# Optimization experiments

Measured on AMD Instinct MI355X. Metric: run time of the kernel, lower is better.

## Reference

```python
import jax, jax.numpy as jnp
import numpy as np

B, L, D = 4, 2048, 512
CHUNK = 64
EPS = 1e-5


def setup_inputs() -> dict:
    key = jax.random.key(0)
    kx, kw = jax.random.split(key)
    x = jax.random.normal(kx, (B, L, D), dtype=jnp.float32)
    W = jax.random.normal(kw, (D, D), dtype=jnp.float32) / np.float32(np.sqrt(D))
    return {
        "x": x,
        "W": W,
        "eta": jnp.asarray(0.01, jnp.float32),
        "lam_logit": jnp.asarray(np.log(0.99 / 0.01), jnp.float32),  # logit(0.99)
        "ln_gamma": jnp.ones((D,), jnp.float32),
        "ln_beta": jnp.zeros((D,), jnp.float32),
    }


def _gated_delta_scan(k, v, q, lam, beta):
    """Gated delta rule: S_t = lam*S_{t-1} + beta * k_t (x) (v_t - lam*S_{t-1}^T k_t);
    o_t = S_t^T q_t (scale=1.0, single head of dim D). k,v,q: [B,L,D] -> o: [B,L,D]."""
    b, l, d = k.shape
    nc = l // CHUNK

    def to_scan(t):  # [B,L,D] -> [nc, CHUNK, B, D]
        return t.transpose(1, 0, 2).reshape(nc, CHUNK, b, d)

    ks, vs, qs = to_scan(k), to_scan(v), to_scan(q)

    def step(S, inp):
        k_t, v_t, q_t = inp                      # each [B,D]
        S = lam * S                              # scalar decay exp(g), g = log(lam)
        v_err = beta * (v_t - jnp.einsum('bk,bkv->bv', k_t, S))
        S = S + k_t[:, :, None] * v_err[:, None, :]
        o_t = jnp.einsum('bk,bkv->bv', q_t, S)
        return S, o_t

    def chunk_body(S, ch):
        return jax.lax.scan(step, S, ch)

    S0 = jnp.zeros((b, d, d), k.dtype)
    _, o = jax.lax.scan(chunk_body, S0, (ks, vs, qs))  # o: [nc, CHUNK, B, D]
    return o.reshape(l, b, d).transpose(1, 0, 2)


def reference(x, W, eta, lam_logit, ln_gamma, ln_beta):
    lam = jax.nn.sigmoid(lam_logit)
    x_act = jnp.tanh(x)
    static_out = jnp.einsum('bld,ed->ble', x_act, W)  # torch Linear (no bias): x @ W.T
    # k = q = tanh(x), v = W @ tanh(x), g = log(lam), beta = eta
    o_dyn = _gated_delta_scan(x_act, static_out, x_act, lam, eta)
    y = static_out + o_dyn
    mu = jnp.mean(y, axis=-1, keepdims=True)
    var = jnp.var(y, axis=-1, keepdims=True)
    return (y - mu) * jax.lax.rsqrt(var + EPS) * ln_gamma + ln_beta
```

## Files before the change

kernel.cpp:

```cpp
#include <hip/hip_runtime.h>
#include <math.h>

#define BB 4
#define LL 2048
#define DD 512
#define CC 64
#define NC 32
#define VB 8
#define EPSF 1e-5f

typedef unsigned int u32;
typedef unsigned short u16;
typedef __attribute__((ext_vector_type(4))) u32 u32x4;
typedef __attribute__((ext_vector_type(4))) float f32x4;
typedef __attribute__((ext_vector_type(8))) __bf16 bf16x8;

__device__ __forceinline__ u16 f2bf(float f) {
  return __builtin_bit_cast(u16, (__bf16)f);
}
__device__ __forceinline__ int sx6(int s) { return (s ^ (s >> 3)) & 7; }
__device__ __forceinline__ bf16x8 ldf(const u16* p) {
  return __builtin_bit_cast(bf16x8, *(const u32x4*)p);
}
__device__ __forceinline__ bf16x8 bcv(u32x4 v) { return __builtin_bit_cast(bf16x8, v); }

__device__ __forceinline__ void gld16(u16* lds, const u16* g) {
  __builtin_amdgcn_global_load_lds(
      (const __attribute__((address_space(1))) u32*)g,
      (__attribute__((address_space(3))) u32*)lds, 16, 0, 0);
}
__device__ __forceinline__ void barrier_lgkm() {
  asm volatile("s_waitcnt lgkmcnt(0)" ::: "memory");
  __builtin_amdgcn_sched_barrier(0);
  __builtin_amdgcn_s_barrier();
  __builtin_amdgcn_sched_barrier(0);
}
__device__ __forceinline__ void barrier_all() {
  asm volatile("s_waitcnt vmcnt(0) lgkmcnt(0)" ::: "memory");
  __builtin_amdgcn_sched_barrier(0);
  __builtin_amdgcn_s_barrier();
  __builtin_amdgcn_sched_barrier(0);
}

__global__ __launch_bounds__(256) void k_pre2(const float* __restrict__ x,
                                              const float* __restrict__ W,
                                              u16* __restrict__ kbs,
                                              u16* __restrict__ wbb,
                                              u16* __restrict__ kbt) {
  __shared__ __align__(16) u16 Ls[16 * 520];
  int blk = blockIdx.x;
  int tid = threadIdx.x;
  if (blk < 512) {
    int bc = blk >> 2;
    int q = blk & 3;
    int b = bc >> 5, c = bc & 31;
    int s0 = q * 16;
    const float* xg = x + (size_t)(b * LL + c * CC + s0) * DD;
    u16* kbs_c = kbs + (size_t)(b * LL + c * CC + s0) * DD;
#pragma unroll
    for (int i = 0; i < 4; ++i) {
      int idx = tid + i * 256;
      int r = idx >> 6, k8 = (idx & 63) * 8;
      const float* xp = xg + (size_t)r * DD + k8;
      float4 a = *(const float4*)xp;
      float4 b4 = *(const float4*)(xp + 4);
      float v[8] = {a.x, a.y, a.z, a.w, b4.x, b4.y, b4.z, b4.w};
      u32x4 pk;
#pragma unroll
      for (int j = 0; j < 4; ++j)
        pk[j] = (u32)f2bf(tanhf(v[2 * j])) | ((u32)f2bf(tanhf(v[2 * j + 1])) << 16);
      int s = s0 + r;
      *(u32x4*)(kbs_c + (size_t)r * DD + (k8 ^ (sx6(s) << 3))) = pk;
      *(u32x4*)&Ls[r * 520 + k8] = pk;
    }
    __syncthreads();
    u16* ktb = kbt + (size_t)bc * CC * DD;
#pragma unroll
    for (int kk = 0; kk < 2; ++kk) {
      int k = tid * 2 + kk;
      int mk = sx6(k) << 3;
#pragma unroll
      for (int g2 = 0; g2 < 2; ++g2) {
        int g = q * 2 + g2;
        u32 w4[4];
#pragma unroll
        for (int p = 0; p < 4; ++p) {
          int sL = g2 * 8 + 2 * p;
          u16 e0 = Ls[sL * 520 + k];
          u16 e1 = Ls[(sL + 1) * 520 + k];
          w4[p] = (u32)e0 | ((u32)e1 << 16);
        }
        *(u32x4*)(ktb + (size_t)k * 64 + ((8 * g) ^ mk)) =
            (u32x4){w4[0], w4[1], w4[2], w4[3]};
      }
    }
  } else {
    int idx = ((blk - 512) * 256 + tid) * 8;
    float4 a = *(const float4*)(W + idx);
    float4 b = *(const float4*)(W + idx + 4);
    float v[8] = {a.x, a.y, a.z, a.w, b.x, b.y, b.z, b.w};
    u32x4 pk;
#pragma unroll
    for (int j = 0; j < 4; ++j)
      pk[j] = (u32)f2bf(v[2 * j]) | ((u32)f2bf(v[2 * j + 1]) << 16);
    *(u32x4*)(wbb + idx) = pk;
  }
}

__global__ __launch_bounds__(512) void k_prep5(const u16* __restrict__ kbs,
                                               const float* __restrict__ eta_p,
                                               const float* __restrict__ ll_p,
                                               u16* __restrict__ tbs,
                                               u16* __restrict__ tcs,
                                               u16* __restrict__ p1g,
                                               u16* __restrict__ p2g) {
  __shared__ __align__(16) u16 Kl[CC * DD];
  __shared__ float Gl[64 * 64];
  __shared__ float Gs[64 * 64];
  __shared__ float Tl[64 * 65];
  __shared__ __align__(16) u16 MtL[64 * 64];
  __shared__ __align__(16) u16 TbT[64 * 64];
  __shared__ __align__(16) u16 TcT[64 * 64];
  __shared__ float pw[72];
  int bc = blockIdx.x;
  int b = bc >> 5, c = bc & 31;
  int tid = threadIdx.x;
  int wid = tid >> 6, lane = tid & 63;
  int wq2 = wid & 3, kh2 = wid >> 2;
  int lo = lane & 15, hi = lane >> 4;
  float beta = *eta_p;
  float lam = 1.f / (1.f + expf(-*ll_p));
  if (tid <= 64) pw[tid] = powf(lam, (float)tid);
  for (int i = tid; i < 64 * 65; i += 512) Tl[i] = 0.f;
  const u16* Kg = kbs + (size_t)(b * LL + c * CC) * DD;
#pragma unroll
  for (int i = 0; i < 8; ++i)
    gld16(Kl + (size_t)(i * 512 + tid) * 8, Kg + (size_t)(i * 512 + tid) * 8);
  __syncthreads();
  {
    f32x4 acc[4] = {{0.f,0.f,0.f,0.f},{0.f,0.f,0.f,0.f},{0.f,0.f,0.f,0.f},{0.f,0.f,0.f,0.f}};
    int t = 16 * wq2 + lo;
    int mT = sx6(t) << 3;
#pragma unroll
    for (int kq = 0; kq < 8; ++kq) {
      int col = kh2 * 256 + hi * 8 + kq * 32;
      bf16x8 aF = ldf(Kl + t * DD + (col ^ mT));
#pragma unroll
      for (int sb = 0; sb < 4; ++sb) {
        int s = 16 * sb + lo;
        bf16x8 bF = ldf(Kl + s * DD + (col ^ (sx6(s) << 3)));
        acc[sb] = __builtin_amdgcn_mfma_f32_16x16x32_bf16(aF, bF, acc[sb], 0, 0, 0);
      }
    }
    float* Gp = kh2 ? Gs : Gl;
#pragma unroll
    for (int sb = 0; sb < 4; ++sb)
#pragma unroll
      for (int r = 0; r < 4; ++r)
        Gp[(16 * wq2 + 4 * hi + r) * 64 + 16 * sb + lo] = acc[sb][r];
  }
  __syncthreads();
#pragma unroll
  for (int i = 0; i < 8; ++i) {
    int idx = tid + i * 512;
    int tq = idx >> 6, sq = idx & 63;
    float g = Gl[idx] + Gs[idx];
    Gl[idx] = g;
    Gs[idx] = (sq < tq) ? beta * pw[tq - sq] * g : 0.f;
  }
  __syncthreads();
  if (tid < 256) {
    int q = hi;
    int j = 16 * wid + lo;
    for (int t = 0; t < 64; ++t) {
      float ps = 0.f;
#pragma unroll
      for (int i = 0; i < 16; ++i) {
        int s = 16 * q + i;
        ps = fmaf(Gs[t * 64 + s], Tl[s * 65 + j], ps);
      }
      ps += __shfl_xor(ps, 16, 64);
      ps += __shfl_xor(ps, 32, 64);
      if (q == 0) Tl[t * 65 + j] = ((t == j) ? 1.f : 0.f) - ps;
    }
  }
  __syncthreads();
  u16* tbso = tbs + (size_t)bc * 4096;
  u16* tcso = tcs + (size_t)bc * 4096;
#pragma unroll
  for (int i = 0; i < 8; ++i) {
    int idx = tid + i * 512;
    int s = idx >> 6, r = idx & 63;
    float tv = Tl[s * 65 + r];
    float sc = pw[63 - s] * beta;
    tbso[idx] = f2bf(sc * tv);
    tcso[idx] = f2bf(-sc * pw[r + 1] * tv);
    int swz = r ^ (sx6(s) << 3);
    float mtv = (r < s) ? pw[s - r] * Gl[s * 64 + r]
                        : ((r == s) ? Gl[s * 64 + r] : 0.f);
    MtL[s * 64 + swz] = f2bf(mtv);
    float tvT = Tl[r * 65 + s];
    TbT[s * 64 + swz] = f2bf(beta * tvT);
    TcT[s * 64 + swz] = f2bf(-beta * pw[s + 1] * tvT);
  }
  __syncthreads();
  {
    f32x4 pa[4];
#pragma unroll
    for (int rt = 0; rt < 4; ++rt) pa[rt] = (f32x4){0.f, 0.f, 0.f, 0.f};
    int srow = 16 * wq2 + lo;
    int aswz = sx6(srow) << 3;
    const u16* Bt = kh2 ? TcT : TbT;
#pragma unroll
    for (int km = 0; km < 2; ++km) {
      int mo = hi * 8 + km * 32;
      bf16x8 aF = ldf(MtL + srow * 64 + (mo ^ aswz));
#pragma unroll
      for (int rt = 0; rt < 4; ++rt) {
        int rrow = 16 * rt + lo;
        int bswz = sx6(rrow) << 3;
        pa[rt] = __builtin_amdgcn_mfma_f32_16x16x32_bf16(
            aF, ldf(Bt + rrow * 64 + (mo ^ bswz)), pa[rt], 0, 0, 0);
      }
    }
    u16* po = (kh2 ? p2g : p1g) + (size_t)bc * 4096;
#pragma unroll
    for (int rt = 0; rt < 4; ++rt)
#pragma unroll
      for (int rg = 0; rg < 4; ++rg) {
        int s = 16 * wq2 + 4 * hi + rg;
        int r = 16 * rt + lo;
        float d = kh2 ? ((s == r) ? pw[s + 1] : 0.f)
                      : ((s == r) ? 1.f : 0.f);
        po[s * 64 + r] = f2bf(pa[rt][rg] + d);
      }
  }
}

__global__ __launch_bounds__(512, 2) void k_scanC(const u16* __restrict__ kbs,
                                                  const u16* __restrict__ kbt,
                                                  const u16* __restrict__ wbb,
                                                  const u16* __restrict__ tbs,
                                                  const u16* __restrict__ tcs,
                                                  const u16* __restrict__ p1g,
                                                  const u16* __restrict__ p2g,
                                                  const float* __restrict__ ll_p,
                                                  float* __restrict__ y) {
  __shared__ __align__(16) u16 Sb[16 * DD];
  __shared__ __align__(16) u16 Ut2[2][16 * 64];
  __shared__ __align__(16) u16 Vt2[2][16 * 64];
  __shared__ __align__(16) u16 Ws[16 * 64];

  int b = blockIdx.x >> 6;
  int vb = blockIdx.x & 63;
  int v0 = vb * VB;
  int tid = threadIdx.x;
  int wid = tid >> 6, lane = tid & 63;
  int wq = wid & 3, kh = wid >> 2;
  int lo = lane & 15, hi = lane >> 4;
  int sidx = 16 * wq + lo;
  int mS = sx6(sidx) << 3;
  int mLo = sx6(lo) << 3;
  int kOff = kh * 256;

  float lam = 1.f / (1.f + expf(-*ll_p));
  float lam64 = powf(lam, 64.f);

  {
    u32x4 z = {0u, 0u, 0u, 0u};
    ((u32x4*)Sb)[tid] = z;
    if (tid < 256) {
      ((u32x4*)Ut2)[tid] = z;
      ((u32x4*)Vt2)[tid] = z;
    }
    if (tid < 128) ((u32x4*)Ws)[tid] = z;
    if (wid < 8) {
      u32x4 wrow = *(const u32x4*)(wbb + (size_t)(v0 + wid) * DD + lane * 8);
      *(u32x4*)(Sb + (size_t)(8 + wid) * DD + ((lane * 8) ^ (sx6(8 + wid) << 3))) = wrow;
    }
  }
  const u16* kb_b = kbs + (size_t)b * LL * DD;
  float* yb = y + (size_t)b * LL * DD;

  u32x4 kB[8];
#pragma unroll
  for (int kq = 0; kq < 8; ++kq)
    kB[kq] = *(const u32x4*)(kb_b + (size_t)sidx * DD +
                             ((kOff + hi * 8 + kq * 32) ^ mS));
  u32x4 kt0[4], kt1[4], fA0, fA1, fB0, fB1;
  {
    const u16* ktc = kbt + (size_t)(b * NC + 0) * CC * DD;
#pragma unroll
    for (int t = 0; t < 4; ++t) {
      int k = 16 * (4 * wid + t) + lo;
      const u16* rowp = ktc + (size_t)k * 64;
      int m = sx6(k) << 3;
      kt0[t] = *(const u32x4*)(rowp + ((8 * hi) ^ m));
      kt1[t] = *(const u32x4*)(rowp + ((8 * hi + 32) ^ m));
    }
    size_t tbase = ((size_t)(b * NC + 0) * 64 + sidx) * 64 + hi * 8;
    const u16* mA = (kh == 0) ? tbs : p1g;
    const u16* mB = (kh == 0) ? tcs : p2g;
    fA0 = *(const u32x4*)(mA + tbase);
    fA1 = *(const u32x4*)(mA + tbase + 32);
    fB0 = *(const u32x4*)(mB + tbase);
    fB1 = *(const u32x4*)(mB + tbase + 32);
  }
  f32x4 Sa[4];
#pragma unroll
  for (int t = 0; t < 4; ++t) Sa[t] = (f32x4){0.f, 0.f, 0.f, 0.f};
  barrier_all();

  for (int c = 0; c < NC; ++c) {
    {
      f32x4 A0 = {0.f,0.f,0.f,0.f}, A1 = {0.f,0.f,0.f,0.f};
#pragma unroll
      for (int kq = 0; kq < 8; ++kq) {
        int col = kOff + hi * 8 + kq * 32;
        bf16x8 sA = ldf(Sb + lo * DD + (col ^ mLo));
        if (kq & 1) A1 = __builtin_amdgcn_mfma_f32_16x16x32_bf16(sA, bcv(kB[kq]), A1, 0, 0, 0);
        else        A0 = __builtin_amdgcn_mfma_f32_16x16x32_bf16(sA, bcv(kB[kq]), A0, 0, 0, 0);
      }
      f32x4 F = A0 + A1;
      if (hi < 2) {
#pragma unroll
        for (int r = 0; r < 4; ++r) {
          int m = 4 * hi + r;
          Ut2[kh][m * 64 + (sidx ^ (sx6(m) << 3))] = f2bf(F[r]);
        }
      } else {
#pragma unroll
        for (int r = 0; r < 4; ++r) {
          int m = 4 * hi + r - 8;
          Vt2[kh][m * 64 + (sidx ^ (sx6(m) << 3))] = f2bf(F[r]);
        }
      }
    }
    if (c + 1 < NC) {
      const u16* src = kb_b + ((size_t)(c + 1) * CC + sidx) * DD;
#pragma unroll
      for (int kq = 0; kq < 8; ++kq)
        kB[kq] = *(const u32x4*)(src + ((kOff + hi * 8 + kq * 32) ^ mS));
    }
    barrier_lgkm();
    {
      f32x4 Wa0 = {0.f,0.f,0.f,0.f}, Wa1 = {0.f,0.f,0.f,0.f};
#pragma unroll
      for (int h = 0; h < 2; ++h) {
        bf16x8 vf0 = ldf(Vt2[h] + lo * 64 + ((hi * 8) ^ mLo));
        bf16x8 vf1 = ldf(Vt2[h] + lo * 64 + ((hi * 8 + 32) ^ mLo));
        bf16x8 uf0 = ldf(Ut2[h] + lo * 64 + ((hi * 8) ^ mLo));
        bf16x8 uf1 = ldf(Ut2[h] + lo * 64 + ((hi * 8 + 32) ^ mLo));
        Wa0 = __builtin_amdgcn_mfma_f32_16x16x32_bf16(vf0, bcv(fA0), Wa0, 0, 0, 0);
        Wa1 = __builtin_amdgcn_mfma_f32_16x16x32_bf16(vf1, bcv(fA1), Wa1, 0, 0, 0);
        Wa0 = __builtin_amdgcn_mfma_f32_16x16x32_bf16(uf0, bcv(fB0), Wa0, 0, 0, 0);
        Wa1 = __builtin_amdgcn_mfma_f32_16x16x32_bf16(uf1, bcv(fB1), Wa1, 0, 0, 0);
      }
      f32x4 Wa = Wa0 + Wa1;
      if (kh == 0) {
        if (hi < 2) {
#pragma unroll
          for (int r = 0; r < 4; ++r) {
            int v = 4 * hi + r;
            Ws[v * 64 + (sidx ^ (sx6(v) << 3))] = f2bf(Wa[r]);
          }
        }
      } else {
        if (hi < 2) {
          float4 yo = make_float4(Wa[0], Wa[1], Wa[2], Wa[3]);
          *(float4*)(yb + (size_t)(c * CC + sidx) * DD + v0 + 4 * hi) = yo;
        }
      }
    }
    barrier_lgkm();
    {
      bf16x8 ws0 = ldf(Ws + lo * 64 + ((hi * 8) ^ mLo));
      bf16x8 ws1 = ldf(Ws + lo * 64 + ((hi * 8 + 32) ^ mLo));
#pragma unroll
      for (int t = 0; t < 4; ++t) {
        f32x4 acc = Sa[t] * lam64;
        acc = __builtin_amdgcn_mfma_f32_16x16x32_bf16(ws0, bcv(kt0[t]), acc, 0, 0, 0);
        acc = __builtin_amdgcn_mfma_f32_16x16x32_bf16(ws1, bcv(kt1[t]), acc, 0, 0, 0);
        Sa[t] = acc;
      }
      if (hi < 2) {
#pragma unroll
        for (int t = 0; t < 4; ++t) {
          int kc = 16 * (4 * wid + t) + lo;
#pragma unroll
          for (int r = 0; r < 4; ++r) {
            int v = 4 * hi + r;
            Sb[v * DD + (kc ^ (sx6(v) << 3))] = f2bf(Sa[t][r]);
          }
        }
      }
    }
    if (c + 1 < NC) {
      const u16* ktc = kbt + (size_t)(b * NC + c + 1) * CC * DD;
#pragma unroll
      for (int t = 0; t < 4; ++t) {
        int k = 16 * (4 * wid + t) + lo;
        const u16* rowp = ktc + (size_t)k * 64;
        int m = sx6(k) << 3;
        kt0[t] = *(const u32x4*)(rowp + ((8 * hi) ^ m));
        kt1[t] = *(const u32x4*)(rowp + ((8 * hi + 32) ^ m));
      }
      size_t tbase = ((size_t)(b * NC + c + 1) * 64 + sidx) * 64 + hi * 8;
      const u16* mA = (kh == 0) ? tbs : p1g;
      const u16* mB = (kh == 0) ? tcs : p2g;
      fA0 = *(const u32x4*)(mA + tbase);
      fA1 = *(const u32x4*)(mA + tbase + 32);
      fB0 = *(const u32x4*)(mB + tbase);
      fB1 = *(const u32x4*)(mB + tbase + 32);
    }
    barrier_lgkm();
  }
}

__global__ __launch_bounds__(256) void k_ln(float* __restrict__ y,
                                            const float* __restrict__ gamma,
                                            const float* __restrict__ lbeta) {
  int row = blockIdx.x * 4 + (threadIdx.x >> 6);
  int lane = threadIdx.x & 63;
  float* yr = y + (size_t)row * DD + lane * 8;
  float4 a = *(const float4*)yr;
  float4 b = *(const float4*)(yr + 4);
  float v[8] = {a.x, a.y, a.z, a.w, b.x, b.y, b.z, b.w};
  float s = 0.f, ss = 0.f;
#pragma unroll
  for (int j = 0; j < 8; ++j) {
    s += v[j];
    ss = fmaf(v[j], v[j], ss);
  }
#pragma unroll
  for (int m = 1; m < 64; m <<= 1) {
    s += __shfl_xor(s, m, 64);
    ss += __shfl_xor(ss, m, 64);
  }
  float mu = s * (1.f / DD);
  float var = ss * (1.f / DD) - mu * mu;
  float inv = rsqrtf(var + EPSF);
  const float* gp = gamma + lane * 8;
  const float* bp = lbeta + lane * 8;
  float4 g0 = *(const float4*)gp;
  float4 g1 = *(const float4*)(gp + 4);
  float4 b0 = *(const float4*)bp;
  float4 b1 = *(const float4*)(bp + 4);
  float g[8] = {g0.x, g0.y, g0.z, g0.w, g1.x, g1.y, g1.z, g1.w};
  float bb[8] = {b0.x, b0.y, b0.z, b0.w, b1.x, b1.y, b1.z, b1.w};
#pragma unroll
  for (int j = 0; j < 8; ++j) v[j] = (v[j] - mu) * inv * g[j] + bb[j];
  *(float4*)yr = make_float4(v[0], v[1], v[2], v[3]);
  *(float4*)(yr + 4) = make_float4(v[4], v[5], v[6], v[7]);
}

extern "C" void kernel_launch(void* const* d_in, const int* in_sizes, int n_in,
                              void* d_out, int out_size, void* d_ws, size_t ws_size,
                              hipStream_t stream) {
  const float* x     = (const float*)d_in[0];
  const float* W     = (const float*)d_in[1];
  const float* eta   = (const float*)d_in[2];
  const float* ll    = (const float*)d_in[3];
  const float* gamma = (const float*)d_in[4];
  const float* lbeta = (const float*)d_in[5];
  float* out = (float*)d_out;

  u16* kbs = (u16*)d_ws;
  u16* kbt = kbs + (size_t)BB * LL * DD;
  u16* wbb = kbt + (size_t)BB * LL * DD;
  u16* tbs = wbb + (size_t)DD * DD;
  u16* tcs = tbs + (size_t)BB * NC * 64 * 64;
  u16* p1g = tcs + (size_t)BB * NC * 64 * 64;
  u16* p2g = p1g + (size_t)BB * NC * 64 * 64;

  k_pre2<<<640, 256, 0, stream>>>(x, W, kbs, wbb, kbt);
  k_prep5<<<BB * NC, 512, 0, stream>>>(kbs, eta, ll, tbs, tcs, p1g, p2g);
  k_scanC<<<256, 512, 0, stream>>>(kbs, kbt, wbb, tbs, tcs, p1g, p2g, ll, out);
  k_ln<<<2048, 256, 0, stream>>>(out, gamma, lbeta);
}
```

Baseline: 131.3 us.

## Process chunk pairs per scan iteration with precomputed cross-chunk correction matrices

The sequential scan now advances two 64-token chunks per iteration. The second chunk's output takes a correction term built from the first chunk's W via extra matrices (tgg/pgg), which the prep kernel computes for odd chunks using a cross-chunk K·K^T product. The state update then runs once per pair with lam^128 decay. This halves the number of serial state updates and their barriers. The cost is more registers, shared memory, prep work and extra bf16 rounding in the correction path.

```diff
diff --git a/kernel.cpp b/kernel.cpp
--- a/kernel.cpp
+++ b/kernel.cpp
@@ -6,6 +6,7 @@
 #define DD 512
 #define CC 64
 #define NC 32
+#define NP 16
 #define VB 8
 #define EPSF 1e-5f
 
@@ -107,13 +108,15 @@
   }
 }
 
-__global__ __launch_bounds__(512) void k_prep5(const u16* __restrict__ kbs,
+__global__ __launch_bounds__(512) void k_prep6(const u16* __restrict__ kbs,
                                                const float* __restrict__ eta_p,
                                                const float* __restrict__ ll_p,
                                                u16* __restrict__ tbs,
                                                u16* __restrict__ tcs,
                                                u16* __restrict__ p1g,
-                                               u16* __restrict__ p2g) {
+                                               u16* __restrict__ p2g,
+                                               u16* __restrict__ tgg,
+                                               u16* __restrict__ pgg) {
   __shared__ __align__(16) u16 Kl[CC * DD];
   __shared__ float Gl[64 * 64];
   __shared__ float Gs[64 * 64];
@@ -122,8 +125,12 @@
   __shared__ __align__(16) u16 TbT[64 * 64];
   __shared__ __align__(16) u16 TcT[64 * 64];
   __shared__ float pw[72];
+  u16* TcsA = (u16*)Gs;
+  u16* GxT  = (u16*)Gs + 4096;
+  u16* P2A  = (u16*)Gl;
   int bc = blockIdx.x;
   int b = bc >> 5, c = bc & 31;
+  int odd = c & 1;
   int tid = threadIdx.x;
   int wid = tid >> 6, lane = tid & 63;
   int wq2 = wid & 3, kh2 = wid >> 2;
@@ -185,6 +192,8 @@
     }
   }
   __syncthreads();
+  float lam64 = pw[64];
+  float cscl = odd ? lam64 : 1.f;
   u16* tbso = tbs + (size_t)bc * 4096;
   u16* tcso = tcs + (size_t)bc * 4096;
 #pragma unroll
@@ -193,8 +202,9 @@
     int s = idx >> 6, r = idx & 63;
     float tv = Tl[s * 65 + r];
     float sc = pw[63 - s] * beta;
+    float tcv = -sc * pw[r + 1] * tv;
     tbso[idx] = f2bf(sc * tv);
-    tcso[idx] = f2bf(-sc * pw[r + 1] * tv);
+    tcso[idx] = f2bf(cscl * tcv);
     int swz = r ^ (sx6(s) << 3);
     float mtv = (r < s) ? pw[s - r] * Gl[s * 64 + r]
                         : ((r == s) ? Gl[s * 64 + r] : 0.f);
@@ -202,6 +212,7 @@
     float tvT = Tl[r * 65 + s];
     TbT[s * 64 + swz] = f2bf(beta * tvT);
     TcT[s * 64 + swz] = f2bf(-beta * pw[s + 1] * tvT);
+    if (odd) TcsA[s * 64 + swz] = f2bf(tcv);
   }
   __syncthreads();
   {
@@ -232,24 +243,89 @@
         int r = 16 * rt + lo;
         float d = kh2 ? ((s == r) ? pw[s + 1] : 0.f)
                       : ((s == r) ? 1.f : 0.f);
-        po[s * 64 + r] = f2bf(pa[rt][rg] + d);
-      }
-  }
-}
-
-__global__ __launch_bounds__(512, 2) void k_scanC(const u16* __restrict__ kbs,
+        float val = pa[rt][rg] + d;
+        po[s * 64 + r] = f2bf(kh2 ? (cscl * val) : val);
+        if (odd && kh2)
+          P2A[s * 64 + ((16 * rt + lo) ^ (sx6(s) << 3))] = f2bf(val);
+      }
+  }
+  if (odd) {
+    const u16* K0g = kbs + (size_t)(b * LL + (c - 1) * CC) * DD;
+#pragma unroll
+    for (int blk2 = 0; blk2 < 2; ++blk2) {
+      int idx = 2 * wid + blk2;
+      int qb = idx >> 2, rb = idx & 3;
+      int qrow = qb * 16 + lo;
+      int rrow = rb * 16 + lo;
+      int mQ = sx6(qrow) << 3;
+      int mR = sx6(rrow) << 3;
+      f32x4 acc = (f32x4){0.f, 0.f, 0.f, 0.f};
+#pragma unroll
+      for (int km = 0; km < 16; ++km) {
+        int col = hi * 8 + km * 32;
+        bf16x8 aF = ldf(Kl + qrow * DD + (col ^ mQ));
+        bf16x8 bF = ldf(K0g + (size_t)rrow * DD + (col ^ mR));
+        acc = __builtin_amdgcn_mfma_f32_16x16x32_bf16(aF, bF, acc, 0, 0, 0);
+      }
+#pragma unroll
+      for (int rr = 0; rr < 4; ++rr) {
+        int qv = qb * 16 + 4 * hi + rr;
+        int rv = rb * 16 + lo;
+        GxT[rv * 64 + (qv ^ (sx6(rv) << 3))] = f2bf(acc[rr]);
+      }
+    }
+    __syncthreads();
+    {
+      f32x4 pa[4];
+#pragma unroll
+      for (int rt = 0; rt < 4; ++rt) pa[rt] = (f32x4){0.f, 0.f, 0.f, 0.f};
+      int srow = 16 * wq2 + lo;
+      int aswz = sx6(srow) << 3;
+      const u16* At = kh2 ? P2A : TcsA;
+#pragma unroll
+      for (int km = 0; km < 2; ++km) {
+        int mo = hi * 8 + km * 32;
+        bf16x8 aF = ldf(At + srow * 64 + (mo ^ aswz));
+#pragma unroll
+        for (int rt = 0; rt < 4; ++rt) {
+          int rrow = 16 * rt + lo;
+          int bswz = sx6(rrow) << 3;
+          pa[rt] = __builtin_amdgcn_mfma_f32_16x16x32_bf16(
+              aF, ldf(GxT + rrow * 64 + (mo ^ bswz)), pa[rt], 0, 0, 0);
+        }
+      }
+      u16* po = (kh2 ? pgg : tgg) + (size_t)(b * NP + (c >> 1)) * 4096;
+#pragma unroll
+      for (int rt = 0; rt < 4; ++rt)
+#pragma unroll
+        for (int rg = 0; rg < 4; ++rg) {
+          int s = 16 * wq2 + 4 * hi + rg;
+          int r = 16 * rt + lo;
+          po[s * 64 + r] = f2bf(pa[rt][rg]);
+        }
+    }
+  }
+}
+
+__global__ __launch_bounds__(512, 2) void k_scanD(const u16* __restrict__ kbs,
                                                   const u16* __restrict__ kbt,
                                                   const u16* __restrict__ wbb,
                                                   const u16* __restrict__ tbs,
                                                   const u16* __restrict__ tcs,
                                                   const u16* __restrict__ p1g,
                                                   const u16* __restrict__ p2g,
+                                                  const u16* __restrict__ tgg,
+                                                  const u16* __restrict__ pgg,
                                                   const float* __restrict__ ll_p,
                                                   float* __restrict__ y) {
   __shared__ __align__(16) u16 Sb[16 * DD];
-  __shared__ __align__(16) u16 Ut2[2][16 * 64];
-  __shared__ __align__(16) u16 Vt2[2][16 * 64];
-  __shared__ __align__(16) u16 Ws[16 * 64];
+  __shared__ __align__(16) u16 Ut0[2][16 * 64];
+  __shared__ __align__(16) u16 Vt0[2][16 * 64];
+  __shared__ __align__(16) u16 Ut1[2][16 * 64];
+  __shared__ __align__(16) u16 Vt1[2][16 * 64];
+  __shared__ __align__(16) u16 Ws0[16 * 64];
+  __shared__ __align__(16) u16 Ws0s[16 * 64];
+  __shared__ __align__(16) u16 Ws1[16 * 64];
 
   int b = blockIdx.x >> 6;
   int vb = blockIdx.x & 63;
@@ -265,15 +341,22 @@
 
   float lam = 1.f / (1.f + expf(-*ll_p));
   float lam64 = powf(lam, 64.f);
+  float lam128 = lam64 * lam64;
 
   {
     u32x4 z = {0u, 0u, 0u, 0u};
     ((u32x4*)Sb)[tid] = z;
     if (tid < 256) {
-      ((u32x4*)Ut2)[tid] = z;
-      ((u32x4*)Vt2)[tid] = z;
-    }
-    if (tid < 128) ((u32x4*)Ws)[tid] = z;
+      ((u32x4*)Ut0)[tid] = z;
+      ((u32x4*)Vt0)[tid] = z;
+      ((u32x4*)Ut1)[tid] = z;
+      ((u32x4*)Vt1)[tid] = z;
+    }
+    if (tid < 128) {
+      ((u32x4*)Ws0)[tid] = z;
+      ((u32x4*)Ws0s)[tid] = z;
+      ((u32x4*)Ws1)[tid] = z;
+    }
     if (wid < 8) {
       u32x4 wrow = *(const u32x4*)(wbb + (size_t)(v0 + wid) * DD + lane * 8);
       *(u32x4*)(Sb + (size_t)(8 + wid) * DD + ((lane * 8) ^ (sx6(8 + wid) << 3))) = wrow;
@@ -282,79 +365,102 @@
   const u16* kb_b = kbs + (size_t)b * LL * DD;
   float* yb = y + (size_t)b * LL * DD;
 
-  u32x4 kB[8];
-#pragma unroll
-  for (int kq = 0; kq < 8; ++kq)
-    kB[kq] = *(const u32x4*)(kb_b + (size_t)sidx * DD +
-                             ((kOff + hi * 8 + kq * 32) ^ mS));
-  u32x4 kt0[4], kt1[4], fA0, fA1, fB0, fB1;
+  u32x4 kB0[8], kB1[8];
+#pragma unroll
+  for (int kq = 0; kq < 8; ++kq) {
+    int col = (kOff + hi * 8 + kq * 32) ^ mS;
+    kB0[kq] = *(const u32x4*)(kb_b + (size_t)sidx * DD + col);
+    kB1[kq] = *(const u32x4*)(kb_b + (size_t)(CC + sidx) * DD + col);
+  }
+  u32x4 kt0a[4], kt0b[4], kt1a[4], kt1b[4];
+  u32x4 f2A0, f2A1, f2B0, f2B1, f3A0, f3A1, f3B0, f3B1, f3G0, f3G1;
   {
-    const u16* ktc = kbt + (size_t)(b * NC + 0) * CC * DD;
+    const u16* kc0 = kbt + (size_t)(b * NC + 0) * CC * DD;
+    const u16* kc1 = kbt + (size_t)(b * NC + 1) * CC * DD;
 #pragma unroll
     for (int t = 0; t < 4; ++t) {
       int k = 16 * (4 * wid + t) + lo;
-      const u16* rowp = ktc + (size_t)k * 64;
       int m = sx6(k) << 3;
-      kt0[t] = *(const u32x4*)(rowp + ((8 * hi) ^ m));
-      kt1[t] = *(const u32x4*)(rowp + ((8 * hi + 32) ^ m));
-    }
-    size_t tbase = ((size_t)(b * NC + 0) * 64 + sidx) * 64 + hi * 8;
-    const u16* mA = (kh == 0) ? tbs : p1g;
-    const u16* mB = (kh == 0) ? tcs : p2g;
-    fA0 = *(const u32x4*)(mA + tbase);
-    fA1 = *(const u32x4*)(mA + tbase + 32);
-    fB0 = *(const u32x4*)(mB + tbase);
-    fB1 = *(const u32x4*)(mB + tbase + 32);
+      kt0a[t] = *(const u32x4*)(kc0 + (size_t)k * 64 + ((8 * hi) ^ m));
+      kt0b[t] = *(const u32x4*)(kc0 + (size_t)k * 64 + ((8 * hi + 32) ^ m));
+      kt1a[t] = *(const u32x4*)(kc1 + (size_t)k * 64 + ((8 * hi) ^ m));
+      kt1b[t] = *(const u32x4*)(kc1 + (size_t)k * 64 + ((8 * hi + 32) ^ m));
+    }
+    size_t t2 = ((size_t)(b * NC + 0) * 64 + sidx) * 64 + hi * 8;
+    size_t t3 = ((size_t)(b * NC + 1) * 64 + sidx) * 64 + hi * 8;
+    size_t tg = ((size_t)(b * NP + 0) * 64 + sidx) * 64 + hi * 8;
+    const u16* mA = kh ? p1g : tbs;
+    const u16* mB = kh ? p2g : tcs;
+    const u16* mG = kh ? pgg : tgg;
+    f2A0 = *(const u32x4*)(mA + t2); f2A1 = *(const u32x4*)(mA + t2 + 32);
+    f2B0 = *(const u32x4*)(mB + t2); f2B1 = *(const u32x4*)(mB + t2 + 32);
+    f3A0 = *(const u32x4*)(mA + t3); f3A1 = *(const u32x4*)(mA + t3 + 32);
+    f3B0 = *(const u32x4*)(mB + t3); f3B1 = *(const u32x4*)(mB + t3 + 32);
+    f3G0 = *(const u32x4*)(mG + tg); f3G1 = *(const u32x4*)(mG + tg + 32);
   }
   f32x4 Sa[4];
 #pragma unroll
   for (int t = 0; t < 4; ++t) Sa[t] = (f32x4){0.f, 0.f, 0.f, 0.f};
   barrier_all();
 
-  for (int c = 0; c < NC; ++c) {
+  for (int p = 0; p < NP; ++p) {
     {
       f32x4 A0 = {0.f,0.f,0.f,0.f}, A1 = {0.f,0.f,0.f,0.f};
+      f32x4 C0 = {0.f,0.f,0.f,0.f}, C1 = {0.f,0.f,0.f,0.f};
 #pragma unroll
       for (int kq = 0; kq < 8; ++kq) {
         int col = kOff + hi * 8 + kq * 32;
         bf16x8 sA = ldf(Sb + lo * DD + (col ^ mLo));
-        if (kq & 1) A1 = __builtin_amdgcn_mfma_f32_16x16x32_bf16(sA, bcv(kB[kq]), A1, 0, 0, 0);
-        else        A0 = __builtin_amdgcn_mfma_f32_16x16x32_bf16(sA, bcv(kB[kq]), A0, 0, 0, 0);
-      }
-      f32x4 F = A0 + A1;
+        if (kq & 1) {
+          A1 = __builtin_amdgcn_mfma_f32_16x16x32_bf16(sA, bcv(kB0[kq]), A1, 0, 0, 0);
+          C1 = __builtin_amdgcn_mfma_f32_16x16x32_bf16(sA, bcv(kB1[kq]), C1, 0, 0, 0);
+        } else {
+          A0 = __builtin_amdgcn_mfma_f32_16x16x32_bf16(sA, bcv(kB0[kq]), A0, 0, 0, 0);
+          C0 = __builtin_amdgcn_mfma_f32_16x16x32_bf16(sA, bcv(kB1[kq]), C0, 0, 0, 0);
+        }
+      }
+      f32x4 F0 = A0 + A1, F1 = C0 + C1;
       if (hi < 2) {
 #pragma unroll
         for (int r = 0; r < 4; ++r) {
           int m = 4 * hi + r;
-          Ut2[kh][m * 64 + (sidx ^ (sx6(m) << 3))] = f2bf(F[r]);
+          int off = m * 64 + (sidx ^ (sx6(m) << 3));
+          Ut0[kh][off] = f2bf(F0[r]);
+          Ut1[kh][off] = f2bf(F1[r]);
         }
       } else {
 #pragma unroll
         for (int r = 0; r < 4; ++r) {
           int m = 4 * hi + r - 8;
-          Vt2[kh][m * 64 + (sidx ^ (sx6(m) << 3))] = f2bf(F[r]);
-        }
-      }
-    }
-    if (c + 1 < NC) {
-      const u16* src = kb_b + ((size_t)(c + 1) * CC + sidx) * DD;
-#pragma unroll
-      for (int kq = 0; kq < 8; ++kq)
-        kB[kq] = *(const u32x4*)(src + ((kOff + hi * 8 + kq * 32) ^ mS));
+          int off = m * 64 + (sidx ^ (sx6(m) << 3));
+          Vt0[kh][off] = f2bf(F0[r]);
+          Vt1[kh][off] = f2bf(F1[r]);
+        }
+      }
+    }
+    if (p + 1 < NP) {
+      const u16* s0 = kb_b + ((size_t)(2 * p + 2) * CC + sidx) * DD;
+      const u16* s1 = kb_b + ((size_t)(2 * p + 3) * CC + sidx) * DD;
+#pragma unroll
+      for (int kq = 0; kq < 8; ++kq) {
+        int col = (kOff + hi * 8 + kq * 32) ^ mS;
+        kB0[kq] = *(const u32x4*)(s0 + col);
+        kB1[kq] = *(const u32x4*)(s1 + col);
+      }
     }
     barrier_lgkm();
     {
       f32x4 Wa0 = {0.f,0.f,0.f,0.f}, Wa1 = {0.f,0.f,0.f,0.f};
 #pragma unroll
       for (int h = 0; h < 2; ++h) {
-        bf16x8 vf0 = ldf(Vt2[h] + lo * 64 + ((hi * 8) ^ mLo));
-        bf16x8 vf1 = ldf(Vt2[h] + lo * 64 + ((hi * 8 + 32) ^ mLo));
-        bf16x8 uf0 = ldf(Ut2[h] + lo * 64 + ((hi * 8) ^ mLo));
-        bf16x8 uf1 = ldf(Ut2[h] + lo * 64 + ((hi * 8 + 32) ^ mLo));
-        Wa0 = __builtin_amdgcn_mfma_f32_16x16x32_bf16(vf0, bcv(fA0), Wa0, 0, 0, 0);
-        Wa1 = __builtin_amdgcn_mfma_f32_16x16x32_bf16(vf1, bcv(fA1), Wa1, 0, 0, 0);
-        Wa0 = __builtin_amdgcn_mfma_f32_16x16x32_bf16(uf0, bcv(fB0), Wa0, 0, 0, 0);
-        Wa1 = __builtin_amdgcn_mfma_f32_16x16x32_bf16(uf1, bcv(fB1), Wa1, 0, 0, 0);
+        bf16x8 vf0 = ldf(Vt0[h] + lo * 64 + ((hi * 8) ^ mLo));
+        bf16x8 vf1 = ldf(Vt0[h] + lo * 64 + ((hi * 8 + 32) ^ mLo));
+        bf16x8 uf0 = ldf(Ut0[h] + lo * 64 + ((hi * 8) ^ mLo));
+        bf16x8 uf1 = ldf(Ut0[h] + lo * 64 + ((hi * 8 + 32) ^ mLo));
+        Wa0 = __builtin_amdgcn_mfma_f32_16x16x32_bf16(vf0, bcv(f2A0), Wa0, 0, 0, 0);
+        Wa1 = __builtin_amdgcn_mfma_f32_16x16x32_bf16(vf1, bcv(f2A1), Wa1, 0, 0, 0);
+        Wa0 = __builtin_amdgcn_mfma_f32_16x16x32_bf16(uf0, bcv(f2B0), Wa0, 0, 0, 0);
+        Wa1 = __builtin_amdgcn_mfma_f32_16x16x32_bf16(uf1, bcv(f2B1), Wa1, 0, 0, 0);
       }
       f32x4 Wa = Wa0 + Wa1;
       if (kh == 0) {
@@ -362,25 +468,63 @@
 #pragma unroll
           for (int r = 0; r < 4; ++r) {
             int v = 4 * hi + r;
-            Ws[v * 64 + (sidx ^ (sx6(v) << 3))] = f2bf(Wa[r]);
+            int off = v * 64 + (sidx ^ (sx6(v) << 3));
+            Ws0[off] = f2bf(Wa[r]);
+            Ws0s[off] = f2bf(Wa[r] * lam64);
           }
         }
-      } else {
-        if (hi < 2) {
-          float4 yo = make_float4(Wa[0], Wa[1], Wa[2], Wa[3]);
-          *(float4*)(yb + (size_t)(c * CC + sidx) * DD + v0 + 4 * hi) = yo;
-        }
+      } else if (hi < 2) {
+        *(float4*)(yb + (size_t)(2 * p * CC + sidx) * DD + v0 + 4 * hi) =
+            make_float4(Wa[0], Wa[1], Wa[2], Wa[3]);
       }
     }
     barrier_lgkm();
     {
-      bf16x8 ws0 = ldf(Ws + lo * 64 + ((hi * 8) ^ mLo));
-      bf16x8 ws1 = ldf(Ws + lo * 64 + ((hi * 8 + 32) ^ mLo));
+      f32x4 Wa0 = {0.f,0.f,0.f,0.f}, Wa1 = {0.f,0.f,0.f,0.f};
+#pragma unroll
+      for (int h = 0; h < 2; ++h) {
+        bf16x8 vf0 = ldf(Vt1[h] + lo * 64 + ((hi * 8) ^ mLo));
+        bf16x8 vf1 = ldf(Vt1[h] + lo * 64 + ((hi * 8 + 32) ^ mLo));
+        bf16x8 uf0 = ldf(Ut1[h] + lo * 64 + ((hi * 8) ^ mLo));
+        bf16x8 uf1 = ldf(Ut1[h] + lo * 64 + ((hi * 8 + 32) ^ mLo));
+        Wa0 = __builtin_amdgcn_mfma_f32_16x16x32_bf16(vf0, bcv(f3A0), Wa0, 0, 0, 0);
+        Wa1 = __builtin_amdgcn_mfma_f32_16x16x32_bf16(vf1, bcv(f3A1), Wa1, 0, 0, 0);
+        Wa0 = __builtin_amdgcn_mfma_f32_16x16x32_bf16(uf0, bcv(f3B0), Wa0, 0, 0, 0);
+        Wa1 = __builtin_amdgcn_mfma_f32_16x16x32_bf16(uf1, bcv(f3B1), Wa1, 0, 0, 0);
+      }
+      {
+        bf16x8 w0 = ldf(Ws0 + lo * 64 + ((hi * 8) ^ mLo));
+        bf16x8 w1 = ldf(Ws0 + lo * 64 + ((hi * 8 + 32) ^ mLo));
+        Wa0 = __builtin_amdgcn_mfma_f32_16x16x32_bf16(w0, bcv(f3G0), Wa0, 0, 0, 0);
+        Wa1 = __builtin_amdgcn_mfma_f32_16x16x32_bf16(w1, bcv(f3G1), Wa1, 0, 0, 0);
+      }
+      f32x4 Wa = Wa0 + Wa1;
+      if (kh == 0) {
+        if (hi < 2) {
+#pragma unroll
+          for (int r = 0; r < 4; ++r) {
+            int v = 4 * hi + r;
+            Ws1[v * 64 + (sidx ^ (sx6(v) << 3))] = f2bf(Wa[r]);
+          }
+        }
+      } else if (hi < 2) {
+        *(float4*)(yb + (size_t)((2 * p + 1) * CC + sidx) * DD + v0 + 4 * hi) =
+            make_float4(Wa[0], Wa[1], Wa[2], Wa[3]);
+      }
+    }
+    barrier_lgkm();
+    {
+      bf16x8 w00 = ldf(Ws0s + lo * 64 + ((hi * 8) ^ mLo));
+      bf16x8 w01 = ldf(Ws0s + lo * 64 + ((hi * 8 + 32) ^ mLo));
+      bf16x8 w10 = ldf(Ws1 + lo * 64 + ((hi * 8) ^ mLo));
+      bf16x8 w11 = ldf(Ws1 + lo * 64 + ((hi * 8 + 32) ^ mLo));
 #pragma unroll
       for (int t = 0; t < 4; ++t) {
-        f32x4 acc = Sa[t] * lam64;
-        acc = __builtin_amdgcn_mfma_f32_16x16x32_bf16(ws0, bcv(kt0[t]), acc, 0, 0, 0);
-        acc = __builtin_amdgcn_mfma_f32_16x16x32_bf16(ws1, bcv(kt1[t]), acc, 0, 0, 0);
+        f32x4 acc = Sa[t] * lam128;
+        acc = __builtin_amdgcn_mfma_f32_16x16x32_bf16(w00, bcv(kt0a[t]), acc, 0, 0, 0);
+        acc = __builtin_amdgcn_mfma_f32_16x16x32_bf16(w01, bcv(kt0b[t]), acc, 0, 0, 0);
+        acc = __builtin_amdgcn_mfma_f32_16x16x32_bf16(w10, bcv(kt1a[t]), acc, 0, 0, 0);
+        acc = __builtin_amdgcn_mfma_f32_16x16x32_bf16(w11, bcv(kt1b[t]), acc, 0, 0, 0);
         Sa[t] = acc;
       }
       if (hi < 2) {
@@ -395,23 +539,29 @@
         }
       }
     }
-    if (c + 1 < NC) {
-      const u16* ktc = kbt + (size_t)(b * NC + c + 1) * CC * DD;
+    if (p + 1 < NP) {
+      const u16* kc0 = kbt + (size_t)(b * NC + 2 * p + 2) * CC * DD;
+      const u16* kc1 = kbt + (size_t)(b * NC + 2 * p + 3) * CC * DD;
 #pragma unroll
       for (int t = 0; t < 4; ++t) {
         int k = 16 * (4 * wid + t) + lo;
-        const u16* rowp = ktc + (size_t)k * 64;
         int m = sx6(k) << 3;
-        kt0[t] = *(const u32x4*)(rowp + ((8 * hi) ^ m));
-        kt1[t] = *(const u32x4*)(rowp + ((8 * hi + 32) ^ m));
-      }
-      size_t tbase = ((size_t)(b * NC + c + 1) * 64 + sidx) * 64 + hi * 8;
-      const u16* mA = (kh == 0) ? tbs : p1g;
-      const u16* mB = (kh == 0) ? tcs : p2g;
-      fA0 = *(const u32x4*)(mA + tbase);
-      fA1 = *(const u32x4*)(mA + tbase + 32);
-      fB0 = *(const u32x4*)(mB + tbase);
-      fB1 = *(const u32x4*)(mB + tbase + 32);
+        kt0a[t] = *(const u32x4*)(kc0 + (size_t)k * 64 + ((8 * hi) ^ m));
+        kt0b[t] = *(const u32x4*)(kc0 + (size_t)k * 64 + ((8 * hi + 32) ^ m));
+        kt1a[t] = *(const u32x4*)(kc1 + (size_t)k * 64 + ((8 * hi) ^ m));
+        kt1b[t] = *(const u32x4*)(kc1 + (size_t)k * 64 + ((8 * hi + 32) ^ m));
+      }
+      size_t t2 = ((size_t)(b * NC + 2 * p + 2) * 64 + sidx) * 64 + hi * 8;
+      size_t t3 = ((size_t)(b * NC + 2 * p + 3) * 64 + sidx) * 64 + hi * 8;
+      size_t tg = ((size_t)(b * NP + p + 1) * 64 + sidx) * 64 + hi * 8;
+      const u16* mA = kh ? p1g : tbs;
+      const u16* mB = kh ? p2g : tcs;
+      const u16* mG = kh ? pgg : tgg;
+      f2A0 = *(const u32x4*)(mA + t2); f2A1 = *(const u32x4*)(mA + t2 + 32);
+      f2B0 = *(const u32x4*)(mB + t2); f2B1 = *(const u32x4*)(mB + t2 + 32);
+      f3A0 = *(const u32x4*)(mA + t3); f3A1 = *(const u32x4*)(mA + t3 + 32);
+      f3B0 = *(const u32x4*)(mB + t3); f3B1 = *(const u32x4*)(mB + t3 + 32);
+      f3G0 = *(const u32x4*)(mG + tg); f3G1 = *(const u32x4*)(mG + tg + 32);
     }
     barrier_lgkm();
   }
@@ -472,9 +622,11 @@
   u16* tcs = tbs + (size_t)BB * NC * 64 * 64;
   u16* p1g = tcs + (size_t)BB * NC * 64 * 64;
   u16* p2g = p1g + (size_t)BB * NC * 64 * 64;
+  u16* tgg = p2g + (size_t)BB * NC * 64 * 64;
+  u16* pgg = tgg + (size_t)BB * NP * 64 * 64;
 
   k_pre2<<<640, 256, 0, stream>>>(x, W, kbs, wbb, kbt);
-  k_prep5<<<BB * NC, 512, 0, stream>>>(kbs, eta, ll, tbs, tcs, p1g, p2g);
-  k_scanC<<<256, 512, 0, stream>>>(kbs, kbt, wbb, tbs, tcs, p1g, p2g, ll, out);
+  k_prep6<<<BB * NC, 512, 0, stream>>>(kbs, eta, ll, tbs, tcs, p1g, p2g, tgg, pgg);
+  k_scanD<<<256, 512, 0, stream>>>(kbs, kbt, wbb, tbs, tcs, p1g, p2g, tgg, pgg, ll, out);
   k_ln<<<2048, 256, 0, stream>>>(out, gamma, lbeta);
 }
```

Measured after the change: 369.9 us. +181.8%, slower.
